# Kernel tuning notes

Measured on AMD Instinct MI355X. Metric: run time of the kernel, lower is better.

## Reference

```python
import jax, jax.numpy as jnp
import numpy as np

B, N, NPOINT, C = 4, 16384, 4096, 64
NSAMPLE = 32


def setup_inputs() -> dict:
    key = jax.random.key(0)
    k1, k2, k3 = jax.random.split(key, 3)
    xyz = jax.random.normal(k1, (B, N, 3), dtype=jnp.float32)
    new_xyz = jax.random.normal(k2, (B, NPOINT, 3), dtype=jnp.float32)
    features = jax.random.normal(k3, (B, C, N), dtype=jnp.float32)
    return {"xyz": xyz, "new_xyz": new_xyz, "features": features, "nsample": NSAMPLE}


def _knn_idx(new_xyz, xyz, k):
    # squared pairwise distances: (B, npoint, N)
    dists = jnp.sum((new_xyz[:, :, None, :] - xyz[:, None, :, :]) ** 2, axis=-1)
    # k smallest distances -> top_k on negated distances (fused top-k instead of full argsort)
    _, idx = jax.lax.top_k(-dists, k)  # (B, npoint, k) int32
    return idx


def reference(xyz, new_xyz, features, nsample):
    idx = _knn_idx(new_xyz, xyz, nsample)  # (B, npoint, nsample)

    # group xyz: (B, npoint, nsample, 3)
    grouped_xyz = jax.vmap(lambda pts, i: pts[i])(xyz, idx)
    # center on the query points and move coords to channel dim: (B, 3, npoint, nsample)
    grouped_xyz = grouped_xyz - new_xyz[:, :, None, :]
    grouped_xyz = jnp.transpose(grouped_xyz, (0, 3, 1, 2))

    # group features: (B, C, npoint, nsample)
    grouped_features = jax.vmap(lambda f, i: f[:, i])(features, idx)

    # use_xyz=True -> concat along channel dim: (B, 3 + C, npoint, nsample)
    new_features = jnp.concatenate([grouped_xyz, grouped_features], axis=1)
    return new_features
```

## Files before the change

kernel.cpp:

```cpp
#include <hip/hip_runtime.h>

#define NBATCH 4
#define NPTS   16384
#define NQ     4096
#define NCH    64
#define K      32
#define CHOUT  67

typedef float v2f __attribute__((ext_vector_type(2)));
typedef float v4f __attribute__((ext_vector_type(4)));
typedef int   v4i __attribute__((ext_vector_type(4)));

__device__ __forceinline__ v2f pk_add(v2f a, v2f b) {
    v2f d; asm("v_pk_add_f32 %0, %1, %2" : "=v"(d) : "v"(a), "v"(b)); return d;
}
__device__ __forceinline__ v2f pk_mul(v2f a, v2f b) {
    v2f d; asm("v_pk_mul_f32 %0, %1, %2" : "=v"(d) : "v"(a), "v"(b)); return d;
}
__device__ __forceinline__ int dpp_shr1(int v) {
    return __builtin_amdgcn_update_dpp(v, v, 0x138, 0xf, 0xf, false);
}
__device__ __forceinline__ int sel_mask_i(unsigned long long m, int t, int f) {
    int d; asm("v_cndmask_b32 %0, %2, %1, %3" : "=v"(d) : "v"(t), "v"(f), "s"(m));
    return d;
}

constexpr int TILE = 1024;
constexpr int QPW  = 2;
constexpr int QPB  = 8;

__global__ __launch_bounds__(256) void knn_kernel(
    const float* __restrict__ xyz,
    const float* __restrict__ new_xyz,
    int*   __restrict__ out_idx,
    float* __restrict__ out)
{
    __shared__ float sx[TILE], sy[TILE], sz[TILE];

    const int tid  = threadIdx.x;
    const int lane = tid & 63;
    const int wave = tid >> 6;
    const int b    = blockIdx.x >> 9;
    const int q0   = (blockIdx.x & 511) * QPB + wave * QPW;

    const float* xb = xyz + (size_t)b * NPTS * 3;

    float nqx[QPW], nqy[QPW], nqz[QPW];
    v2f nqx2[QPW], nqy2[QPW], nqz2[QPW];
#pragma unroll
    for (int j = 0; j < QPW; ++j) {
        const int base = ((b * NQ) + q0 + j) * 3;
        nqx[j] = __int_as_float(__builtin_amdgcn_readfirstlane(__float_as_int(-new_xyz[base + 0])));
        nqy[j] = __int_as_float(__builtin_amdgcn_readfirstlane(__float_as_int(-new_xyz[base + 1])));
        nqz[j] = __int_as_float(__builtin_amdgcn_readfirstlane(__float_as_int(-new_xyz[base + 2])));
        nqx2[j] = (v2f){nqx[j], nqx[j]};
        nqy2[j] = (v2f){nqy[j], nqy[j]};
        nqz2[j] = (v2f){nqz[j], nqz[j]};
    }

    const float INF  = __int_as_float(0x7f800000);
    const float NINF = __int_as_float(0xff800000);

    float vmA[QPW], vmB[QPW];
#pragma unroll
    for (int j = 0; j < QPW; ++j) { vmA[j] = INF; vmB[j] = INF; }

    for (int t0 = 0; t0 < NPTS; t0 += TILE) {
        __syncthreads();
        for (int i = tid; i < TILE; i += 256) {
            const float* s = xb + (size_t)(t0 + i) * 3;
            sx[i] = s[0]; sy[i] = s[1]; sz[i] = s[2];
        }
        __syncthreads();

#pragma unroll 2
        for (int ii = 0; ii < TILE / 2; ii += 64) {
            const int i = ii + lane;
            const v2f px2 = *(const v2f*)(sx + 2 * i);
            const v2f py2 = *(const v2f*)(sy + 2 * i);
            const v2f pz2 = *(const v2f*)(sz + 2 * i);
#pragma unroll
            for (int j = 0; j < QPW; ++j) {
                const v2f dx = pk_add(px2, nqx2[j]);
                const v2f dy = pk_add(py2, nqy2[j]);
                const v2f dz = pk_add(pz2, nqz2[j]);
                const v2f d2 = pk_add(pk_add(pk_mul(dx, dx), pk_mul(dy, dy)),
                                      pk_mul(dz, dz));
                vmA[j] = fminf(vmA[j], d2.x);
                vmB[j] = fminf(vmB[j], d2.y);
            }
        }
    }

    float Tf[QPW];
#pragma unroll
    for (int j = 0; j < QPW; ++j) {
        const unsigned u = __float_as_uint(fminf(vmA[j], vmB[j]));
        unsigned t = 0x7fffffffu;
        for (int bb = 30; bb >= 0; --bb) {
            const unsigned tt = t ^ (1u << bb);
            const int cnt = __popcll(__ballot(u <= tt));
            if (cnt >= 32) t = tt;
        }
        Tf[j] = __uint_as_float(t);
    }

    float ld[QPW]; int li[QPW];
#pragma unroll
    for (int j = 0; j < QPW; ++j) {
        ld[j] = (lane < K) ? INF : NINF;
        li[j] = 0;
    }

    for (int t0 = 0; t0 < NPTS; t0 += TILE) {
        __syncthreads();
        for (int i = tid; i < TILE; i += 256) {
            const float* s = xb + (size_t)(t0 + i) * 3;
            sx[i] = s[0]; sy[i] = s[1]; sz[i] = s[2];
        }
        __syncthreads();

#pragma unroll 2
        for (int ii = 0; ii < TILE / 2; ii += 64) {
            const int i = ii + lane;
            const v2f px2 = *(const v2f*)(sx + 2 * i);
            const v2f py2 = *(const v2f*)(sy + 2 * i);
            const v2f pz2 = *(const v2f*)(sz + 2 * i);
            const int ibase = t0 + 2 * ii;
#pragma unroll
            for (int j = 0; j < QPW; ++j) {
                const v2f dx = pk_add(px2, nqx2[j]);
                const v2f dy = pk_add(py2, nqy2[j]);
                const v2f dz = pk_add(pz2, nqz2[j]);
                const v2f d2 = pk_add(pk_add(pk_mul(dx, dx), pk_mul(dy, dy)),
                                      pk_mul(dz, dz));
                unsigned long long m0 = __ballot(d2.x <= Tf[j]);
                unsigned long long m1 = __ballot(d2.y <= Tf[j]);
                while (m0 | m1) {
                    const int c0 = m0 ? (int)__builtin_ctzll(m0) : 64;
                    const int c1 = m1 ? (int)__builtin_ctzll(m1) : 64;
                    const bool lo = c0 <= c1;
                    const int c = lo ? c0 : c1;
                    if (lo) m0 &= m0 - 1; else m1 &= m1 - 1;
                    const int b0 = __builtin_amdgcn_readlane(__float_as_int(d2.x), c);
                    const int b1 = __builtin_amdgcn_readlane(__float_as_int(d2.y), c);
                    const float dn = __int_as_float(lo ? b0 : b1);
                    const int cand = ibase + 2 * c + (lo ? 0 : 1);
                    const unsigned long long sh = __ballot(ld[j] > dn);
                    const int p = sh ? (int)__builtin_ctzll(sh) : 64;
                    const int sld = dpp_shr1(__float_as_int(ld[j]));
                    const int sli = dpp_shr1(li[j]);
                    const int nld = sel_mask_i(sh, sld, __float_as_int(ld[j]));
                    const int nli = sel_mask_i(sh, sli, li[j]);
                    ld[j] = __int_as_float((lane == p) ? __float_as_int(dn) : nld);
                    li[j] = (lane == p) ? cand : nli;
                }
            }
        }
    }

#pragma unroll
    for (int j = 0; j < QPW; ++j) {
        if (lane < K) {
            const int q   = q0 + j;
            const int idx = li[j];
            out_idx[((size_t)(b * NQ) + q) * K + lane] = idx;
            const float px = xb[idx * 3 + 0];
            const float py = xb[idx * 3 + 1];
            const float pz = xb[idx * 3 + 2];
            const size_t plane = (size_t)NQ * K;
            const size_t o = (((size_t)b * CHOUT + 0) * NQ + q) * K + lane;
            out[o]             = __fadd_rn(px, nqx[j]);
            out[o + plane]     = __fadd_rn(py, nqy[j]);
            out[o + 2 * plane] = __fadd_rn(pz, nqz[j]);
        }
    }
}

__global__ __launch_bounds__(1024) void gather_kernel(
    const float* __restrict__ features,
    const int*   __restrict__ idx,
    float* __restrict__ out)
{
    __shared__ __align__(16) float row[NPTS];

    const int tid  = threadIdx.x;
    const int half = blockIdx.x & 1;
    const int c    = (blockIdx.x >> 1) & 63;
    const int b    = blockIdx.x >> 7;

    const v4f* src = (const v4f*)(features + ((size_t)(b * NCH + c)) * NPTS);
    for (int k2 = tid; k2 < NPTS / 4; k2 += 1024) ((v4f*)row)[k2] = src[k2];
    __syncthreads();

    const size_t hofs = (size_t)half * (NQ * K / 2);
    const v4i* gi = (const v4i*)(idx + (size_t)b * NQ * K + hofs);
    v4f* dst = (v4f*)(out + ((size_t)(b * CHOUT + 3 + c)) * NQ * K + hofs);

    v4i cur = gi[tid];
#pragma unroll
    for (int it = 0; it < 16; ++it) {
        v4i nxt;
        if (it < 15) nxt = gi[tid + (it + 1) * 1024];
        v4f o;
        o.x = row[cur.x]; o.y = row[cur.y]; o.z = row[cur.z]; o.w = row[cur.w];
        dst[tid + it * 1024] = o;
        cur = nxt;
    }
}

extern "C" void kernel_launch(void* const* d_in, const int* in_sizes, int n_in,
                              void* d_out, int out_size, void* d_ws, size_t ws_size,
                              hipStream_t stream) {
    const float* xyz      = (const float*)d_in[0];
    const float* new_xyz  = (const float*)d_in[1];
    const float* features = (const float*)d_in[2];
    float* out    = (float*)d_out;
    int*   ws_idx = (int*)d_ws;

    knn_kernel<<<dim3(NBATCH * (NQ / QPB)), dim3(256), 0, stream>>>(xyz, new_xyz, ws_idx, out);
    gather_kernel<<<dim3(NBATCH * NCH * 2), dim3(1024), 0, stream>>>(features, ws_idx, out);
}
```

Before: 306.7 us.

## Pipeline xyz tiles via async LDS loads and gather features from transposed layout

The KNN kernel now stages xyz tiles straight into a triple-buffered LDS ring with global_load_lds and explicit waitcnt/barrier calls, so loading the next tiles overlaps distance computation. The first pass also uses packed FMA. A new transpose kernel writes features in point-major order, and a new gather kernel reads contiguous 64-channel rows per neighbour and writes output through LDS. The threshold gets a small ULP slack to absorb FMA rounding differences between the two passes. This adds an extra kernel and workspace traffic and depends on the workspace being large enough; otherwise the old path runs.

```diff
diff --git a/kernel.cpp b/kernel.cpp
--- a/kernel.cpp
+++ b/kernel.cpp
@@ -17,6 +17,9 @@
 __device__ __forceinline__ v2f pk_mul(v2f a, v2f b) {
     v2f d; asm("v_pk_mul_f32 %0, %1, %2" : "=v"(d) : "v"(a), "v"(b)); return d;
 }
+__device__ __forceinline__ v2f pk_fma(v2f a, v2f b, v2f c) {
+    v2f d; asm("v_pk_fma_f32 %0, %1, %2, %3" : "=v"(d) : "v"(a), "v"(b), "v"(c)); return d;
+}
 __device__ __forceinline__ int dpp_shr1(int v) {
     return __builtin_amdgcn_update_dpp(v, v, 0x138, 0xf, 0xf, false);
 }
@@ -26,8 +29,13 @@
 }
 
 constexpr int TILE = 1024;
+constexpr int NT   = NPTS / TILE;
 constexpr int QPW  = 2;
 constexpr int QPB  = 8;
+
+#define VW3 asm volatile("s_waitcnt vmcnt(3)" ::: "memory")
+#define VW0 asm volatile("s_waitcnt vmcnt(0)" ::: "memory")
+#define BAR __builtin_amdgcn_s_barrier()
 
 __global__ __launch_bounds__(256) void knn_kernel(
     const float* __restrict__ xyz,
@@ -35,7 +43,7 @@
     int*   __restrict__ out_idx,
     float* __restrict__ out)
 {
-    __shared__ float sx[TILE], sy[TILE], sz[TILE];
+    __shared__ __align__(16) float sb[3][TILE * 3];
 
     const int tid  = threadIdx.x;
     const int lane = tid & 63;
@@ -44,6 +52,18 @@
     const int q0   = (blockIdx.x & 511) * QPB + wave * QPW;
 
     const float* xb = xyz + (size_t)b * NPTS * 3;
+    const char* gbase = (const char*)xb + wave * 3072 + lane * 16;
+
+    auto STAGE = [&](int buf, int t0) {
+        const char* g = gbase + (size_t)t0 * 12;
+        char* l = (char*)(&sb[buf][0]) + wave * 3072;
+#define GLL(k) __builtin_amdgcn_global_load_lds( \
+        (const __attribute__((address_space(1))) unsigned int*)(g + (k) * 1024), \
+        (__attribute__((address_space(3))) unsigned int*)(l + (k) * 1024), \
+        16, 0, 0)
+        GLL(0); GLL(1); GLL(2);
+#undef GLL
+    };
 
     float nqx[QPW], nqy[QPW], nqz[QPW];
     v2f nqx2[QPW], nqy2[QPW], nqz2[QPW];
@@ -65,32 +85,42 @@
 #pragma unroll
     for (int j = 0; j < QPW; ++j) { vmA[j] = INF; vmB[j] = INF; }
 
-    for (int t0 = 0; t0 < NPTS; t0 += TILE) {
-        __syncthreads();
-        for (int i = tid; i < TILE; i += 256) {
-            const float* s = xb + (size_t)(t0 + i) * 3;
-            sx[i] = s[0]; sy[i] = s[1]; sz[i] = s[2];
+    STAGE(0, 0);
+    STAGE(1, TILE);
+    VW3; BAR;
+    {
+        int cur = 0, pre = 2;
+        for (int t = 0; t < NT; ++t) {
+            if (t + 2 < NT) STAGE(pre, (t + 2) * TILE);
+            const float* sp = &sb[cur][0];
+#pragma unroll
+            for (int ii = 0; ii < TILE / 128; ++ii) {
+                const float* qp = sp + 3 * (ii * 128 + lane);
+                const v2f px2 = {qp[0], qp[192]};
+                const v2f py2 = {qp[1], qp[193]};
+                const v2f pz2 = {qp[2], qp[194]};
+#pragma unroll
+                for (int j = 0; j < QPW; ++j) {
+                    const v2f dx = pk_add(px2, nqx2[j]);
+                    const v2f dy = pk_add(py2, nqy2[j]);
+                    const v2f dz = pk_add(pz2, nqz2[j]);
+                    const v2f d2 = pk_fma(dx, dx, pk_fma(dy, dy, pk_mul(dz, dz)));
+                    vmA[j] = fminf(vmA[j], d2.x);
+                    vmB[j] = fminf(vmB[j], d2.y);
+                }
+            }
+            if (t + 1 < NT) {
+                if (t + 2 < NT) { VW3; } else { VW0; }
+                BAR;
+            }
+            cur = (cur == 2) ? 0 : cur + 1;
+            pre = (pre == 2) ? 0 : pre + 1;
         }
-        __syncthreads();
-
-#pragma unroll 2
-        for (int ii = 0; ii < TILE / 2; ii += 64) {
-            const int i = ii + lane;
-            const v2f px2 = *(const v2f*)(sx + 2 * i);
-            const v2f py2 = *(const v2f*)(sy + 2 * i);
-            const v2f pz2 = *(const v2f*)(sz + 2 * i);
-#pragma unroll
-            for (int j = 0; j < QPW; ++j) {
-                const v2f dx = pk_add(px2, nqx2[j]);
-                const v2f dy = pk_add(py2, nqy2[j]);
-                const v2f dz = pk_add(pz2, nqz2[j]);
-                const v2f d2 = pk_add(pk_add(pk_mul(dx, dx), pk_mul(dy, dy)),
-                                      pk_mul(dz, dz));
-                vmA[j] = fminf(vmA[j], d2.x);
-                vmB[j] = fminf(vmB[j], d2.y);
-            }
-        }
-    }
+    }
+    BAR;
+
+    STAGE(0, 0);
+    STAGE(1, TILE);
 
     float Tf[QPW];
 #pragma unroll
@@ -102,7 +132,7 @@
             const int cnt = __popcll(__ballot(u <= tt));
             if (cnt >= 32) t = tt;
         }
-        Tf[j] = __uint_as_float(t);
+        Tf[j] = __uint_as_float(t + 64);
     }
 
     float ld[QPW]; int li[QPW];
@@ -112,50 +142,55 @@
         li[j] = 0;
     }
 
-    for (int t0 = 0; t0 < NPTS; t0 += TILE) {
-        __syncthreads();
-        for (int i = tid; i < TILE; i += 256) {
-            const float* s = xb + (size_t)(t0 + i) * 3;
-            sx[i] = s[0]; sy[i] = s[1]; sz[i] = s[2];
-        }
-        __syncthreads();
-
-#pragma unroll 2
-        for (int ii = 0; ii < TILE / 2; ii += 64) {
-            const int i = ii + lane;
-            const v2f px2 = *(const v2f*)(sx + 2 * i);
-            const v2f py2 = *(const v2f*)(sy + 2 * i);
-            const v2f pz2 = *(const v2f*)(sz + 2 * i);
-            const int ibase = t0 + 2 * ii;
-#pragma unroll
-            for (int j = 0; j < QPW; ++j) {
-                const v2f dx = pk_add(px2, nqx2[j]);
-                const v2f dy = pk_add(py2, nqy2[j]);
-                const v2f dz = pk_add(pz2, nqz2[j]);
-                const v2f d2 = pk_add(pk_add(pk_mul(dx, dx), pk_mul(dy, dy)),
-                                      pk_mul(dz, dz));
-                unsigned long long m0 = __ballot(d2.x <= Tf[j]);
-                unsigned long long m1 = __ballot(d2.y <= Tf[j]);
-                while (m0 | m1) {
-                    const int c0 = m0 ? (int)__builtin_ctzll(m0) : 64;
-                    const int c1 = m1 ? (int)__builtin_ctzll(m1) : 64;
-                    const bool lo = c0 <= c1;
-                    const int c = lo ? c0 : c1;
-                    if (lo) m0 &= m0 - 1; else m1 &= m1 - 1;
-                    const int b0 = __builtin_amdgcn_readlane(__float_as_int(d2.x), c);
-                    const int b1 = __builtin_amdgcn_readlane(__float_as_int(d2.y), c);
-                    const float dn = __int_as_float(lo ? b0 : b1);
-                    const int cand = ibase + 2 * c + (lo ? 0 : 1);
-                    const unsigned long long sh = __ballot(ld[j] > dn);
-                    const int p = sh ? (int)__builtin_ctzll(sh) : 64;
-                    const int sld = dpp_shr1(__float_as_int(ld[j]));
-                    const int sli = dpp_shr1(li[j]);
-                    const int nld = sel_mask_i(sh, sld, __float_as_int(ld[j]));
-                    const int nli = sel_mask_i(sh, sli, li[j]);
-                    ld[j] = __int_as_float((lane == p) ? __float_as_int(dn) : nld);
-                    li[j] = (lane == p) ? cand : nli;
+    VW3; BAR;
+    {
+        int cur = 0, pre = 2;
+        for (int t = 0; t < NT; ++t) {
+            if (t + 2 < NT) STAGE(pre, (t + 2) * TILE);
+            const int t0 = t * TILE;
+            const float* sp = &sb[cur][0];
+#pragma unroll
+            for (int ii = 0; ii < TILE / 128; ++ii) {
+                const int gb = t0 + ii * 128;
+                const float* qp = sp + 3 * (ii * 128 + lane);
+                const v2f px2 = {qp[0], qp[192]};
+                const v2f py2 = {qp[1], qp[193]};
+                const v2f pz2 = {qp[2], qp[194]};
+#pragma unroll
+                for (int j = 0; j < QPW; ++j) {
+                    const v2f dx = pk_add(px2, nqx2[j]);
+                    const v2f dy = pk_add(py2, nqy2[j]);
+                    const v2f dz = pk_add(pz2, nqz2[j]);
+                    const v2f d2 = pk_add(pk_add(pk_mul(dx, dx), pk_mul(dy, dy)),
+                                          pk_mul(dz, dz));
+                    unsigned long long m0 = __ballot(d2.x <= Tf[j]);
+                    unsigned long long m1 = __ballot(d2.y <= Tf[j]);
+                    while (m0 | m1) {
+                        const bool lo = (m0 != 0);
+                        const unsigned long long mm = lo ? m0 : m1;
+                        const int c = (int)__builtin_ctzll(mm);
+                        if (lo) m0 &= m0 - 1; else m1 &= m1 - 1;
+                        const int b0 = __builtin_amdgcn_readlane(__float_as_int(d2.x), c);
+                        const int b1 = __builtin_amdgcn_readlane(__float_as_int(d2.y), c);
+                        const float dn = __int_as_float(lo ? b0 : b1);
+                        const int cand = gb + (lo ? 0 : 64) + c;
+                        const unsigned long long sh = __ballot(ld[j] > dn);
+                        const int p = sh ? (int)__builtin_ctzll(sh) : 64;
+                        const int sld = dpp_shr1(__float_as_int(ld[j]));
+                        const int sli = dpp_shr1(li[j]);
+                        const int nld = sel_mask_i(sh, sld, __float_as_int(ld[j]));
+                        const int nli = sel_mask_i(sh, sli, li[j]);
+                        ld[j] = __int_as_float((lane == p) ? __float_as_int(dn) : nld);
+                        li[j] = (lane == p) ? cand : nli;
+                    }
                 }
             }
+            if (t + 1 < NT) {
+                if (t + 2 < NT) { VW3; } else { VW0; }
+                BAR;
+            }
+            cur = (cur == 2) ? 0 : cur + 1;
+            pre = (pre == 2) ? 0 : pre + 1;
         }
     }
 
@@ -177,6 +212,68 @@
     }
 }
 
+__global__ __launch_bounds__(256) void transpose_kernel(
+    const float* __restrict__ f, float* __restrict__ ft)
+{
+    __shared__ float sm[128][65];
+    const int tid = threadIdx.x;
+    const int nb  = blockIdx.x & (NPTS / 128 - 1);
+    const int b   = blockIdx.x >> 7;
+    const int n0  = nb * 128;
+    const float* fb = f + (size_t)b * NCH * NPTS;
+    const int nn = tid & 127, chh = tid >> 7;
+#pragma unroll
+    for (int c = 0; c < NCH; c += 2)
+        sm[nn][c + chh] = fb[(size_t)(c + chh) * NPTS + n0 + nn];
+    __syncthreads();
+    float* ftb = ft + ((size_t)b * NPTS + n0) * NCH;
+#pragma unroll
+    for (int g = 0; g < 32; ++g) {
+        const int o = g * 256 + tid;
+        ftb[o] = sm[o >> 6][o & 63];
+    }
+}
+
+__global__ __launch_bounds__(256) void gather2_kernel(
+    const float* __restrict__ ft,
+    const int*   __restrict__ idx,
+    float* __restrict__ out)
+{
+    __shared__ float smc[NCH][129];
+
+    const int tid = threadIdx.x;
+    const int qt  = blockIdx.x & (NQ / 4 - 1);
+    const int b   = blockIdx.x >> 10;
+    const size_t slot0 = ((size_t)b * NQ + (size_t)qt * 4) * K;
+
+    const int s = tid >> 1;
+    const int h = tid & 1;
+    const int p = idx[slot0 + s];
+    const v4f* src = (const v4f*)(ft + ((size_t)b * NPTS + p) * NCH) + h * 8;
+    v4f r[8];
+#pragma unroll
+    for (int k = 0; k < 8; ++k) r[k] = src[k];
+#pragma unroll
+    for (int k = 0; k < 8; ++k) {
+        const int c0 = h * 32 + k * 4;
+        smc[c0 + 0][s] = r[k].x;
+        smc[c0 + 1][s] = r[k].y;
+        smc[c0 + 2][s] = r[k].z;
+        smc[c0 + 3][s] = r[k].w;
+    }
+    __syncthreads();
+
+    const int w = tid >> 6, l = tid & 63;
+    const size_t plane = (size_t)NQ * K;
+    float* ob = out + ((size_t)b * CHOUT + 3) * plane + (size_t)qt * (4 * K);
+#pragma unroll
+    for (int c = w; c < NCH; c += 4) {
+        float* orow = ob + (size_t)c * plane;
+        orow[l]      = smc[c][l];
+        orow[64 + l] = smc[c][64 + l];
+    }
+}
+
 __global__ __launch_bounds__(1024) void gather_kernel(
     const float* __restrict__ features,
     const int*   __restrict__ idx,
@@ -218,6 +315,16 @@
     float* out    = (float*)d_out;
     int*   ws_idx = (int*)d_ws;
 
-    knn_kernel<<<dim3(NBATCH * (NQ / QPB)), dim3(256), 0, stream>>>(xyz, new_xyz, ws_idx, out);
-    gather_kernel<<<dim3(NBATCH * NCH * 2), dim3(1024), 0, stream>>>(features, ws_idx, out);
-}
+    const size_t idx_bytes = (size_t)NBATCH * NQ * K * sizeof(int);
+    const size_t ft_bytes  = (size_t)NBATCH * NPTS * NCH * sizeof(float);
+    float* featT = (float*)((char*)d_ws + idx_bytes);
+
+    if (ws_size >= idx_bytes + ft_bytes) {
+        transpose_kernel<<<dim3(NBATCH * (NPTS / 128)), dim3(256), 0, stream>>>(features, featT);
+        knn_kernel<<<dim3(NBATCH * (NQ / QPB)), dim3(256), 0, stream>>>(xyz, new_xyz, ws_idx, out);
+        gather2_kernel<<<dim3(NBATCH * (NQ / 4)), dim3(256), 0, stream>>>(featT, ws_idx, out);
+    } else {
+        knn_kernel<<<dim3(NBATCH * (NQ / QPB)), dim3(256), 0, stream>>>(xyz, new_xyz, ws_idx, out);
+        gather_kernel<<<dim3(NBATCH * NCH * 2), dim3(1024), 0, stream>>>(features, ws_idx, out);
+    }
+}
```

New measurement: 338.1 us. +10.2%, slower.
